# Kernel optimization log

Hardware: AMD Instinct MI355X
Metric: run time of the kernel (lower is better)

The kernel has to match this reference:

```python
import jax, jax.numpy as jnp
import numpy as np

N_NODES = 50000
N_EDGES = 800000
IN_CH = 128
HID = 128


def setup_inputs() -> dict:
    key = jax.random.key(0)
    ks = jax.random.split(key, 8)
    s = 0.05
    x = jax.random.normal(ks[0], (N_NODES, IN_CH), dtype=jnp.float32)
    edge_index = jax.random.randint(ks[1], (2, N_EDGES), 0, N_NODES, dtype=jnp.int64)
    W1l = jax.random.normal(ks[2], (IN_CH, HID), dtype=jnp.float32) * s
    W1r = jax.random.normal(ks[3], (IN_CH, HID), dtype=jnp.float32) * s
    b1 = jnp.zeros((HID,), dtype=jnp.float32)
    W2l = jax.random.normal(ks[4], (HID, HID), dtype=jnp.float32) * s
    W2r = jax.random.normal(ks[5], (HID, HID), dtype=jnp.float32) * s
    b2 = jnp.zeros((HID,), dtype=jnp.float32)
    Wout = jax.random.normal(ks[6], (HID, 2), dtype=jnp.float32) * s
    bout = jnp.zeros((2,), dtype=jnp.float32)
    return {"x": x, "edge_index": edge_index, "W1l": W1l, "W1r": W1r, "b1": b1,
            "W2l": W2l, "W2r": W2r, "b2": b2, "Wout": Wout, "bout": bout}


def _mean_aggr(h, src, dst, n_nodes):
    # mean of neighbor (source) features per destination node (PyG SAGEConv default)
    msg_sum = jax.ops.segment_sum(h[src], dst, num_segments=n_nodes)  # [N, D]
    deg = jax.ops.segment_sum(jnp.ones((src.shape[0],), dtype=h.dtype), dst,
                              num_segments=n_nodes)  # [N]
    return msg_sum / jnp.maximum(deg, 1.0)[:, None]


def _sage_conv(h, src, dst, Wl, Wr, b, n_nodes):
    aggr = _mean_aggr(h, src, dst, n_nodes)
    return aggr @ Wl + h @ Wr + b


def reference(x, edge_index, W1l, W1r, b1, W2l, W2r, b2, Wout, bout):
    n = x.shape[0]
    src, dst = edge_index[0], edge_index[1]
    h = jax.nn.relu(_sage_conv(x, src, dst, W1l, W1r, b1, n))
    # dropout is identity in inference mode
    h = jax.nn.relu(_sage_conv(h, src, dst, W2l, W2r, b2, n))
    logits = h @ Wout + bout
    return (logits, h)
```

## Files before the change

### kernel.cpp

```cpp
#include <hip/hip_runtime.h>

#define NN 50000
#define NE 800000
#define CH 128
#define CAP 64
#define PSTRIDE 6256

#define EPT 8
#define ECHUNK (256 * EPT)
#define NCHUNK2 ((NE + ECHUNK - 1) / ECHUNK)
#define EDGE_BLK2 (NCHUNK2 * 8)
#define WTP_BLK 256
#define CAST_BLK ((NN * (CH / 2) / 4 + 255) / 256)

typedef __attribute__((ext_vector_type(8))) short short8;
typedef __attribute__((ext_vector_type(4))) float float4a;
typedef __attribute__((ext_vector_type(4))) int   intx4;
typedef __attribute__((ext_vector_type(4))) float fltx4;
typedef __attribute__((ext_vector_type(4))) unsigned untx4;

#define DEG_OFF  0
#define CSR_OFF  50048
#define XB_OFF   1650048
#define AGB_OFF  4850048
#define H1B_OFF  8050048
#define WTP_OFF  11250048

static __device__ __forceinline__ unsigned short f2b(float f) {
    unsigned u = __float_as_uint(f);
    unsigned r = u + 0x7fff + ((u >> 16) & 1);
    return (unsigned short)(r >> 16);
}

static __device__ __forceinline__ void edge_one(
    int src, int dst, int p, int* __restrict__ deg,
    unsigned short* __restrict__ csr) {
    if ((unsigned)dst < NN && (dst & 7) == p && (unsigned)src < NN) {
        int r = atomicAdd(&deg[p * PSTRIDE + (dst >> 3)], 1);
        r = min(r, CAP - 1);
        csr[(size_t)dst * CAP + r] = (unsigned short)src;
    }
}

__global__ __launch_bounds__(256) void k_build(
    const int* __restrict__ eidx, int* __restrict__ deg,
    unsigned short* __restrict__ csr,
    const float* __restrict__ W1l, const float* __restrict__ W1r,
    const float* __restrict__ W2l, const float* __restrict__ W2r,
    unsigned short* __restrict__ wtp,
    const float* __restrict__ x, unsigned* __restrict__ xb) {
    int b = blockIdx.x;
    if (b < EDGE_BLK2) {
        int p = b & 7;
        int e0 = (b >> 3) * ECHUNK + threadIdx.x * EPT;
        if (e0 < NE) {
            if (e0 + EPT <= NE) {
                intx4 d0 = __builtin_nontemporal_load((const intx4*)(eidx + NE + e0));
                intx4 d1 = __builtin_nontemporal_load((const intx4*)(eidx + NE + e0 + 4));
                intx4 s0 = __builtin_nontemporal_load((const intx4*)(eidx + e0));
                intx4 s1 = __builtin_nontemporal_load((const intx4*)(eidx + e0 + 4));
                edge_one(s0.x, d0.x, p, deg, csr);
                edge_one(s0.y, d0.y, p, deg, csr);
                edge_one(s0.z, d0.z, p, deg, csr);
                edge_one(s0.w, d0.w, p, deg, csr);
                edge_one(s1.x, d1.x, p, deg, csr);
                edge_one(s1.y, d1.y, p, deg, csr);
                edge_one(s1.z, d1.z, p, deg, csr);
                edge_one(s1.w, d1.w, p, deg, csr);
            } else {
                for (int k = 0; k < EPT && e0 + k < NE; ++k)
                    edge_one(eidx[e0 + k], eidx[NE + e0 + k], p, deg, csr);
            }
        }
    } else if (b < EDGE_BLK2 + WTP_BLK) {
        int i = (b - EDGE_BLK2) * 256 + threadIdx.x;
        int layer = i >> 15;
        int li = i & 32767;
        int e = li & 7, lane = (li >> 3) & 63, j = (li >> 9) & 7, kt = li >> 12;
        int ln = lane & 15, quad = lane >> 4;
        int n = j * 16 + ln;
        int k = kt * 32 + quad * 8 + e;
        const float* Wl = layer ? W2l : W1l;
        const float* Wr = layer ? W2r : W1r;
        float v = (k < 128) ? Wl[k * 128 + n] : Wr[(k - 128) * 128 + n];
        __builtin_nontemporal_store(f2b(v), &wtp[(size_t)layer * 32768 + li]);
    } else {
        int gid = (b - EDGE_BLK2 - WTP_BLK) * 256 + threadIdx.x;
        if (gid < NN * (CH / 2) / 4) {
            fltx4 v0 = __builtin_nontemporal_load((const fltx4*)x + gid * 2);
            fltx4 v1 = __builtin_nontemporal_load((const fltx4*)x + gid * 2 + 1);
            untx4 o;
            o.x = (unsigned)f2b(v0.x) | ((unsigned)f2b(v0.y) << 16);
            o.y = (unsigned)f2b(v0.z) | ((unsigned)f2b(v0.w) << 16);
            o.z = (unsigned)f2b(v1.x) | ((unsigned)f2b(v1.y) << 16);
            o.w = (unsigned)f2b(v1.z) | ((unsigned)f2b(v1.w) << 16);
            __builtin_nontemporal_store(o, (untx4*)xb + gid);
        }
    }
}

static __device__ __forceinline__ void acc8(float* acc, uint4 v) {
    acc[0] += __uint_as_float(v.x << 16); acc[1] += __uint_as_float(v.x & 0xffff0000u);
    acc[2] += __uint_as_float(v.y << 16); acc[3] += __uint_as_float(v.y & 0xffff0000u);
    acc[4] += __uint_as_float(v.z << 16); acc[5] += __uint_as_float(v.z & 0xffff0000u);
    acc[6] += __uint_as_float(v.w << 16); acc[7] += __uint_as_float(v.w & 0xffff0000u);
}

__global__ __launch_bounds__(256) void k_gather4(
    const int* __restrict__ deg, const unsigned short* __restrict__ csr,
    const uint4* __restrict__ featb, uint4* __restrict__ aggrb) {
    int wave = (blockIdx.x * 256 + threadIdx.x) >> 6;
    int lane = threadIdx.x & 63;
    if (wave >= NN) return;
    int d = min(deg[(wave & 7) * PSTRIDE + (wave >> 3)], CAP);
    const unsigned short* row = csr + (size_t)wave * CAP;
    int g = lane >> 4;
    int c = lane & 15;

    float acc[8];
    #pragma unroll
    for (int e = 0; e < 8; ++e) acc[e] = 0.0f;

    int i0 = 0;
    for (; i0 + 16 <= d; i0 += 16) {
        int s1 = row[i0 + g];
        int s2 = row[i0 + 4 + g];
        int s3 = row[i0 + 8 + g];
        int s4 = row[i0 + 12 + g];
        uint4 v1 = featb[(size_t)s1 * 16 + c];
        uint4 v2 = featb[(size_t)s2 * 16 + c];
        uint4 v3 = featb[(size_t)s3 * 16 + c];
        uint4 v4 = featb[(size_t)s4 * 16 + c];
        acc8(acc, v1); acc8(acc, v2); acc8(acc, v3); acc8(acc, v4);
    }
    for (; i0 + 8 <= d; i0 += 8) {
        int s1 = row[i0 + g];
        int s2 = row[i0 + 4 + g];
        uint4 v1 = featb[(size_t)s1 * 16 + c];
        uint4 v2 = featb[(size_t)s2 * 16 + c];
        acc8(acc, v1); acc8(acc, v2);
    }
    if (i0 < d) {
        int n1 = i0 + g, n2 = i0 + 4 + g;
        int s1 = (n1 < d) ? (int)row[n1] : 0;
        int s2 = (n2 < d) ? (int)row[n2] : 0;
        uint4 v1 = featb[(size_t)s1 * 16 + c];
        uint4 v2 = featb[(size_t)s2 * 16 + c];
        if (n1 < d) acc8(acc, v1);
        if (n2 < d) acc8(acc, v2);
    }

    #pragma unroll
    for (int e = 0; e < 8; ++e) {
        acc[e] += __shfl_xor(acc[e], 32, 64);
        acc[e] += __shfl_xor(acc[e], 16, 64);
    }
    if (lane < 16) {
        float s = 1.0f / (float)(d > 1 ? d : 1);
        uint4 o;
        o.x = (unsigned)f2b(acc[0] * s) | ((unsigned)f2b(acc[1] * s) << 16);
        o.y = (unsigned)f2b(acc[2] * s) | ((unsigned)f2b(acc[3] * s) << 16);
        o.z = (unsigned)f2b(acc[4] * s) | ((unsigned)f2b(acc[5] * s) << 16);
        o.w = (unsigned)f2b(acc[6] * s) | ((unsigned)f2b(acc[7] * s) << 16);
        aggrb[(size_t)wave * 16 + c] = o;
    }
}

template <bool BF16OUT>
__global__ __launch_bounds__(256) void k_layer_mfma(
    const short* __restrict__ aggrb, const short* __restrict__ hinb,
    const short* __restrict__ wtp, const float* __restrict__ bias,
    float* __restrict__ outf, unsigned short* __restrict__ outb,
    const float* __restrict__ Wout, const float* __restrict__ bout,
    float* __restrict__ logits) {
    int lane = threadIdx.x & 63;
    int wid = threadIdx.x >> 6;
    int m0 = blockIdx.x * 64 + wid * 16;
    int ln = lane & 15;
    int quad = lane >> 4;
    int m = m0 + ln;
    int mc = min(m, NN - 1);

    float4a acc[8];
    #pragma unroll
    for (int j = 0; j < 8; ++j) acc[j] = (float4a){0.0f, 0.0f, 0.0f, 0.0f};

    #pragma unroll
    for (int kt = 0; kt < 8; ++kt) {
        const short* arow = (kt < 4 ? aggrb : hinb) + (size_t)mc * CH + (kt & 3) * 32 + quad * 8;
        short8 av = *(const short8*)arow;
        const short* bk = wtp + (size_t)kt * 4096 + lane * 8;
        #pragma unroll
        for (int j = 0; j < 8; ++j) {
            short8 bv = *(const short8*)(bk + j * 512);
            acc[j] = __builtin_amdgcn_mfma_f32_16x16x32_bf16(av, bv, acc[j], 0, 0, 0);
        }
    }

    float p0[4], p1[4];
    #pragma unroll
    for (int r = 0; r < 4; ++r) { p0[r] = 0.0f; p1[r] = 0.0f; }

    #pragma unroll
    for (int j = 0; j < 8; ++j) {
        int col = j * 16 + ln;
        float bj = bias[col];
        float w0 = 0.0f, w1 = 0.0f;
        if (!BF16OUT) { w0 = Wout[col * 2]; w1 = Wout[col * 2 + 1]; }
        #pragma unroll
        for (int r = 0; r < 4; ++r) {
            int row = m0 + quad * 4 + r;
            float v = fmaxf(acc[j][r] + bj, 0.0f);
            if (row < NN) {
                if (BF16OUT) outb[(size_t)row * CH + col] = f2b(v);
                else         outf[(size_t)row * CH + col] = v;
            }
            if (!BF16OUT) { p0[r] = fmaf(v, w0, p0[r]); p1[r] = fmaf(v, w1, p1[r]); }
        }
    }

    if (!BF16OUT) {
        #pragma unroll
        for (int r = 0; r < 4; ++r) {
            #pragma unroll
            for (int off = 1; off < 16; off <<= 1) {
                p0[r] += __shfl_xor(p0[r], off, 64);
                p1[r] += __shfl_xor(p1[r], off, 64);
            }
        }
        if (ln == 0) {
            float b0 = bout[0], b1 = bout[1];
            #pragma unroll
            for (int r = 0; r < 4; ++r) {
                int row = m0 + quad * 4 + r;
                if (row < NN) {
                    logits[row * 2 + 0] = p0[r] + b0;
                    logits[row * 2 + 1] = p1[r] + b1;
                }
            }
        }
    }
}

extern "C" void kernel_launch(void* const* d_in, const int* in_sizes, int n_in,
                              void* d_out, int out_size, void* d_ws, size_t ws_size,
                              hipStream_t stream) {
    const float* x    = (const float*)d_in[0];
    const int*   eidx = (const int*)d_in[1];
    const float* W1l  = (const float*)d_in[2];
    const float* W1r  = (const float*)d_in[3];
    const float* b1   = (const float*)d_in[4];
    const float* W2l  = (const float*)d_in[5];
    const float* W2r  = (const float*)d_in[6];
    const float* b2   = (const float*)d_in[7];
    const float* Wout = (const float*)d_in[8];
    const float* bout = (const float*)d_in[9];

    float* out    = (float*)d_out;
    float* ws     = (float*)d_ws;
    int*   deg    = (int*)ws;
    unsigned short* csr = (unsigned short*)(ws + CSR_OFF);
    unsigned* xb  = (unsigned*)(ws + XB_OFF);
    unsigned* agb = (unsigned*)(ws + AGB_OFF);
    unsigned* h1b = (unsigned*)(ws + H1B_OFF);
    unsigned short* wtp = (unsigned short*)(ws + WTP_OFF);
    float* logits = out;
    float* hout   = out + 100000;

    (void)hipMemsetAsync(deg, 0, 8 * PSTRIDE * sizeof(int), stream);

    k_build<<<EDGE_BLK2 + WTP_BLK + CAST_BLK, 256, 0, stream>>>(
        eidx, deg, csr, W1l, W1r, W2l, W2r, wtp, x, xb);

    k_gather4<<<(NN + 3) / 4, 256, 0, stream>>>(deg, csr, (const uint4*)xb, (uint4*)agb);
    k_layer_mfma<true><<<(NN + 63) / 64, 256, 0, stream>>>(
        (const short*)agb, (const short*)xb, (const short*)wtp, b1,
        nullptr, (unsigned short*)h1b, nullptr, nullptr, nullptr);

    k_gather4<<<(NN + 3) / 4, 256, 0, stream>>>(deg, csr, (const uint4*)h1b, (uint4*)agb);
    k_layer_mfma<false><<<(NN + 63) / 64, 256, 0, stream>>>(
        (const short*)agb, (const short*)h1b, (const short*)(wtp + 32768), b2,
        hout, nullptr, Wout, bout, logits);
}
```

Before: 241.9 us.

## Split edge CSR build into its own kernel without partition-filtered passes

Result: slower. 254.7 us (+5.3%).

```diff
diff --git a/kernel.cpp b/kernel.cpp
--- a/kernel.cpp
+++ b/kernel.cpp
@@ -6,16 +6,13 @@
 #define CAP 64
 #define PSTRIDE 6256
 
-#define EPT 8
-#define ECHUNK (256 * EPT)
-#define NCHUNK2 ((NE + ECHUNK - 1) / ECHUNK)
-#define EDGE_BLK2 (NCHUNK2 * 8)
+#define EPT2 2
+#define EDGE_GRID ((NE + 256 * EPT2 - 1) / (256 * EPT2))
 #define WTP_BLK 256
 #define CAST_BLK ((NN * (CH / 2) / 4 + 255) / 256)
 
 typedef __attribute__((ext_vector_type(8))) short short8;
 typedef __attribute__((ext_vector_type(4))) float float4a;
-typedef __attribute__((ext_vector_type(4))) int   intx4;
 typedef __attribute__((ext_vector_type(4))) float fltx4;
 typedef __attribute__((ext_vector_type(4))) unsigned untx4;
 
@@ -33,47 +30,35 @@
 }
 
 static __device__ __forceinline__ void edge_one(
-    int src, int dst, int p, int* __restrict__ deg,
+    int src, int dst, int* __restrict__ deg,
     unsigned short* __restrict__ csr) {
-    if ((unsigned)dst < NN && (dst & 7) == p && (unsigned)src < NN) {
+    if ((unsigned)dst < NN && (unsigned)src < NN) {
+        int p = dst & 7;
         int r = atomicAdd(&deg[p * PSTRIDE + (dst >> 3)], 1);
         r = min(r, CAP - 1);
         csr[(size_t)dst * CAP + r] = (unsigned short)src;
     }
 }
 
-__global__ __launch_bounds__(256) void k_build(
+__global__ __launch_bounds__(256) void k_edge(
     const int* __restrict__ eidx, int* __restrict__ deg,
-    unsigned short* __restrict__ csr,
+    unsigned short* __restrict__ csr) {
+    int e0 = (blockIdx.x * 256 + threadIdx.x) * EPT2;
+    if (e0 >= NE) return;
+    int2 s = *(const int2*)(eidx + e0);
+    int2 d = *(const int2*)(eidx + NE + e0);
+    edge_one(s.x, d.x, deg, csr);
+    edge_one(s.y, d.y, deg, csr);
+}
+
+__global__ __launch_bounds__(256) void k_prep(
     const float* __restrict__ W1l, const float* __restrict__ W1r,
     const float* __restrict__ W2l, const float* __restrict__ W2r,
     unsigned short* __restrict__ wtp,
     const float* __restrict__ x, unsigned* __restrict__ xb) {
     int b = blockIdx.x;
-    if (b < EDGE_BLK2) {
-        int p = b & 7;
-        int e0 = (b >> 3) * ECHUNK + threadIdx.x * EPT;
-        if (e0 < NE) {
-            if (e0 + EPT <= NE) {
-                intx4 d0 = __builtin_nontemporal_load((const intx4*)(eidx + NE + e0));
-                intx4 d1 = __builtin_nontemporal_load((const intx4*)(eidx + NE + e0 + 4));
-                intx4 s0 = __builtin_nontemporal_load((const intx4*)(eidx + e0));
-                intx4 s1 = __builtin_nontemporal_load((const intx4*)(eidx + e0 + 4));
-                edge_one(s0.x, d0.x, p, deg, csr);
-                edge_one(s0.y, d0.y, p, deg, csr);
-                edge_one(s0.z, d0.z, p, deg, csr);
-                edge_one(s0.w, d0.w, p, deg, csr);
-                edge_one(s1.x, d1.x, p, deg, csr);
-                edge_one(s1.y, d1.y, p, deg, csr);
-                edge_one(s1.z, d1.z, p, deg, csr);
-                edge_one(s1.w, d1.w, p, deg, csr);
-            } else {
-                for (int k = 0; k < EPT && e0 + k < NE; ++k)
-                    edge_one(eidx[e0 + k], eidx[NE + e0 + k], p, deg, csr);
-            }
-        }
-    } else if (b < EDGE_BLK2 + WTP_BLK) {
-        int i = (b - EDGE_BLK2) * 256 + threadIdx.x;
+    if (b < WTP_BLK) {
+        int i = b * 256 + threadIdx.x;
         int layer = i >> 15;
         int li = i & 32767;
         int e = li & 7, lane = (li >> 3) & 63, j = (li >> 9) & 7, kt = li >> 12;
@@ -85,7 +70,7 @@
         float v = (k < 128) ? Wl[k * 128 + n] : Wr[(k - 128) * 128 + n];
         __builtin_nontemporal_store(f2b(v), &wtp[(size_t)layer * 32768 + li]);
     } else {
-        int gid = (b - EDGE_BLK2 - WTP_BLK) * 256 + threadIdx.x;
+        int gid = (b - WTP_BLK) * 256 + threadIdx.x;
         if (gid < NN * (CH / 2) / 4) {
             fltx4 v0 = __builtin_nontemporal_load((const fltx4*)x + gid * 2);
             fltx4 v1 = __builtin_nontemporal_load((const fltx4*)x + gid * 2 + 1);
@@ -269,8 +254,8 @@
 
     (void)hipMemsetAsync(deg, 0, 8 * PSTRIDE * sizeof(int), stream);
 
-    k_build<<<EDGE_BLK2 + WTP_BLK + CAST_BLK, 256, 0, stream>>>(
-        eidx, deg, csr, W1l, W1r, W2l, W2r, wtp, x, xb);
+    k_edge<<<EDGE_GRID, 256, 0, stream>>>(eidx, deg, csr);
+    k_prep<<<WTP_BLK + CAST_BLK, 256, 0, stream>>>(W1l, W1r, W2l, W2r, wtp, x, xb);
 
     k_gather4<<<(NN + 3) / 4, 256, 0, stream>>>(deg, csr, (const uint4*)xb, (uint4*)agb);
     k_layer_mfma<true><<<(NN + 63) / 64, 256, 0, stream>>>(
```
